# Performance work log

Measured on AMD Instinct MI355X. Metric: run time of the kernel, lower is better.

## Reference

```python
import jax, jax.numpy as jnp
import numpy as np

N = 50000          # nodes
E = 800000         # edges (before self-loops)
IN = 128           # in_dim
HID = 128          # hidden_dim
HEADS = 4
G = 256            # graphs in batch
EPS = 1e-5         # batchnorm eps
NEG_SLOPE = 0.2    # GATConv leaky_relu slope


def _gat_layer(x, src, dst, W, a_src, a_dst, bias, H, C, concat):
    """PyG-style GATConv (self-loops already appended to src/dst)."""
    n = x.shape[0]
    h = (x @ W).reshape(n, H, C)                       # [N,H,C]
    s_src = (h * a_src).sum(-1)                        # [N,H]
    s_dst = (h * a_dst).sum(-1)                        # [N,H]
    e = jax.nn.leaky_relu(s_src[src] + s_dst[dst], NEG_SLOPE)   # [E',H]
    m = jax.ops.segment_max(e, dst, num_segments=n)    # segment-wise softmax
    ex = jnp.exp(e - m[dst])
    den = jax.ops.segment_sum(ex, dst, num_segments=n)
    alpha = ex / den[dst]                              # [E',H]
    out = jax.ops.segment_sum(alpha[..., None] * h[src], dst, num_segments=n)  # [N,H,C]
    out = out.reshape(n, H * C) if concat else out.mean(axis=1)
    return out + bias


def _bn(x, gamma, beta):
    # PyG BatchNorm over nodes (training-mode batch statistics)
    mu = x.mean(axis=0)
    var = x.var(axis=0)
    return gamma * (x - mu) * jax.lax.rsqrt(var + EPS) + beta


def setup_inputs() -> dict:
    key = jax.random.key(0)
    ks = jax.random.split(key, 32)
    d = {}
    d["x"] = jax.random.normal(ks[0], (N, IN), dtype=jnp.float32)
    d["edge_index"] = jax.random.randint(ks[1], (2, E), 0, N, dtype=jnp.int64)
    d["batch_idx"] = jnp.sort(jax.random.randint(ks[2], (N,), 0, G, dtype=jnp.int64))
    dims = [(IN, HEADS, HID, True), (HID * HEADS, HEADS, HID, True), (HID * HEADS, 1, HID, False)]
    for i, (din, H, C, concat) in enumerate(dims):
        d[f"W{i}"] = jax.random.normal(ks[3 + 4 * i], (din, H * C), dtype=jnp.float32) * 0.05
        d[f"att_src{i}"] = jax.random.normal(ks[4 + 4 * i], (H, C), dtype=jnp.float32) * 0.05
        d[f"att_dst{i}"] = jax.random.normal(ks[5 + 4 * i], (H, C), dtype=jnp.float32) * 0.05
        out_w = H * C if concat else C
        d[f"bias{i}"] = jnp.zeros((out_w,), dtype=jnp.float32)
        d[f"gamma{i}"] = jnp.ones((out_w,), dtype=jnp.float32)
        d[f"beta{i}"] = jnp.zeros((out_w,), dtype=jnp.float32)
    return d


def reference(x, edge_index, batch_idx,
              W0, att_src0, att_dst0, bias0, gamma0, beta0,
              W1, att_src1, att_dst1, bias1, gamma1, beta1,
              W2, att_src2, att_dst2, bias2, gamma2, beta2):
    n = x.shape[0]
    loops = jnp.arange(n, dtype=edge_index.dtype)
    src = jnp.concatenate([edge_index[0], loops])
    dst = jnp.concatenate([edge_index[1], loops])
    layers = [
        (W0, att_src0, att_dst0, bias0, gamma0, beta0, HEADS, HID, True),
        (W1, att_src1, att_dst1, bias1, gamma1, beta1, HEADS, HID, True),
        (W2, att_src2, att_dst2, bias2, gamma2, beta2, 1, HID, False),
    ]
    h = x
    for (W, a_s, a_d, b, g, bt, H, C, concat) in layers:
        h = _gat_layer(h, src, dst, W, a_s, a_d, b, H, C, concat)
        h = jax.nn.elu(_bn(h, g, bt))
        # dropout: identity in eval mode
    # global_mean_pool over batch_idx
    sums = jax.ops.segment_sum(h, batch_idx, num_segments=G)
    cnt = jax.ops.segment_sum(jnp.ones((n,), dtype=h.dtype), batch_idx, num_segments=G)
    return sums / jnp.maximum(cnt, 1.0)[:, None]
```

## Files before the change

### kernel.cpp

```cpp
#include <hip/hip_runtime.h>
#include <math.h>
#include <stdint.h>

#define N_NODES 50000
#define N_EDGES 800000
#define EP      (N_EDGES + N_NODES)
#define G_GRAPHS 256
#define BN_EPS   1e-5f
#define NEG_SLOPE 0.2f

typedef short short8 __attribute__((ext_vector_type(8)));
typedef float f32x4 __attribute__((ext_vector_type(4)));
typedef unsigned short u16;

static __device__ __forceinline__ float lrelu(float x) {
    return x > 0.f ? x : NEG_SLOPE * x;
}

static __device__ __forceinline__ u16 bf16hi(float f) {
    unsigned u = __float_as_uint(f);
    u += 0x7FFFu + ((u >> 16) & 1u);
    return (u16)(u >> 16);
}
static __device__ __forceinline__ float bf2f(u16 h) {
    return __uint_as_float((unsigned)h << 16);
}

static __device__ __forceinline__ void gld_lds16(const void* g, void* l) {
    __builtin_amdgcn_global_load_lds((const __attribute__((address_space(1))) void*)g,
                                     (__attribute__((address_space(3))) void*)l, 16, 0, 0);
}

static __device__ __forceinline__ float2 h2f2(unsigned u) {
    union { unsigned u; _Float16 h[2]; } c;
    c.u = u;
    return make_float2((float)c.h[0], (float)c.h[1]);
}

__global__ void k_hist(const int* __restrict__ ei, int* __restrict__ deg) {
    int stride = gridDim.x * blockDim.x;
    for (int e = blockIdx.x * blockDim.x + threadIdx.x; e < EP; e += stride) {
        int d = (e < N_EDGES) ? ei[N_EDGES + e] : (e - N_EDGES);
        atomicAdd(&deg[d], 1);
    }
}

__global__ void k_scan1(const int* __restrict__ deg, int* __restrict__ row_start,
                        int* __restrict__ totals) {
    __shared__ int buf[1024];
    int t = threadIdx.x;
    int i = blockIdx.x * 1024 + t;
    int v = (i < N_NODES) ? deg[i] : 0;
    buf[t] = v;
    __syncthreads();
    for (int off = 1; off < 1024; off <<= 1) {
        int add = (t >= off) ? buf[t - off] : 0;
        __syncthreads();
        buf[t] += add;
        __syncthreads();
    }
    if (i < N_NODES) row_start[i] = buf[t] - v;
    if (t == 1023) totals[blockIdx.x] = buf[t];
}

__global__ void k_scan2(int* __restrict__ totals, int nb) {
    if (threadIdx.x == 0 && blockIdx.x == 0) {
        int run = 0;
        for (int i = 0; i < nb; ++i) { int v = totals[i]; totals[i] = run; run += v; }
    }
}

__global__ void k_scan3(int* __restrict__ row_start, const int* __restrict__ totals) {
    int i = blockIdx.x * blockDim.x + threadIdx.x;
    if (i < N_NODES) row_start[i] += totals[i >> 10];
    if (i == 0) row_start[N_NODES] = EP;
}

__global__ void k_scatter(const int* __restrict__ ei, const int* __restrict__ row_start,
                          int* __restrict__ cursor, int* __restrict__ csr_src) {
    int stride = gridDim.x * blockDim.x;
    for (int e = blockIdx.x * blockDim.x + threadIdx.x; e < EP; e += stride) {
        int s, d;
        if (e < N_EDGES) { s = ei[e]; d = ei[N_EDGES + e]; }
        else             { s = d = e - N_EDGES; }
        int pos = row_start[d] + atomicAdd(&cursor[d], 1);
        csr_src[pos] = s;
    }
}

__global__ void k_cvtW(const float* __restrict__ W, u16* __restrict__ bthi,
                       u16* __restrict__ btlo, int Nc, int nsh, int KS) {
    int i = blockIdx.x * 256 + threadIdx.x;
    if (i >= (KS << 5) * Nc) return;
    int k = i >> nsh;
    int n = i & (Nc - 1);
    int c = n >> 7, col = n & 127;
    int ks = k >> 5, kq = (k >> 3) & 3, j = k & 7;
    size_t idx = ((size_t)(c * KS + ks)) * 4096 + kq * 1024 + col * 8 + j;
    float v = W[i];
    u16 h = bf16hi(v);
    bthi[idx] = h;
    btlo[idx] = bf16hi(v - bf2f(h));
}

__launch_bounds__(256)
__global__ void k_gemm_mfma(const float* __restrict__ A, const u16* __restrict__ bthi,
                            const u16* __restrict__ btlo, _Float16* __restrict__ C2,
                            float* __restrict__ sSg, float* __restrict__ sDg,
                            const float* __restrict__ asr, const float* __restrict__ adr,
                            int M, int K, int Nc) {
    __shared__ u16 Ah[4096], Al[4096], Bh[4096], Bl[4096];
    __shared__ float rS[128], rD[128];
    const int t    = threadIdx.x;
    const int lane = t & 63, wv = t >> 6;
    const int wr = wv >> 1, wc = wv & 1;
    const int lr = lane & 15, kq = lane >> 4;
    const int r0 = blockIdx.x * 128, c0 = blockIdx.y * 128;
    const int KS = K >> 5;
    const int H = Nc >> 7;
    const int head = blockIdx.y;

    const int ar = t >> 1;
    const int ahf = t & 1;
    const int garow = r0 + ar;
    const bool avalid = garow < M;
    const float* arow = A + (size_t)garow * K + ahf * 16;

    const size_t bchunk0 = (size_t)blockIdx.y * KS * 4096;

    f32x4 acc[4][4];
    #pragma unroll
    for (int m = 0; m < 4; ++m)
        #pragma unroll
        for (int n = 0; n < 4; ++n) {
            acc[m][n][0] = 0.f; acc[m][n][1] = 0.f;
            acc[m][n][2] = 0.f; acc[m][n][3] = 0.f;
        }

    for (int ks = 0; ks < KS; ++ks) {
        float4 av[4];
        const float4* ap = (const float4*)(arow + ks * 32);
        if (avalid) {
            av[0] = ap[0]; av[1] = ap[1]; av[2] = ap[2]; av[3] = ap[3];
        } else {
            av[0] = av[1] = av[2] = av[3] = make_float4(0.f, 0.f, 0.f, 0.f);
        }
        __syncthreads();

        float f[16];
        f[0]=av[0].x; f[1]=av[0].y; f[2]=av[0].z; f[3]=av[0].w;
        f[4]=av[1].x; f[5]=av[1].y; f[6]=av[1].z; f[7]=av[1].w;
        f[8]=av[2].x; f[9]=av[2].y; f[10]=av[2].z; f[11]=av[2].w;
        f[12]=av[3].x; f[13]=av[3].y; f[14]=av[3].z; f[15]=av[3].w;
        u16 hi[16], lo[16];
        #pragma unroll
        for (int i = 0; i < 16; ++i) {
            hi[i] = bf16hi(f[i]);
            lo[i] = bf16hi(f[i] - bf2f(hi[i]));
        }
        #pragma unroll
        for (int q = 0; q < 2; ++q) {
            int kqi = ahf * 2 + q;
            int off = kqi * 1024 + ar * 8;
            int4 wh, wl;
            wh.x = (unsigned)hi[q*8+0] | ((unsigned)hi[q*8+1] << 16);
            wh.y = (unsigned)hi[q*8+2] | ((unsigned)hi[q*8+3] << 16);
            wh.z = (unsigned)hi[q*8+4] | ((unsigned)hi[q*8+5] << 16);
            wh.w = (unsigned)hi[q*8+6] | ((unsigned)hi[q*8+7] << 16);
            wl.x = (unsigned)lo[q*8+0] | ((unsigned)lo[q*8+1] << 16);
            wl.y = (unsigned)lo[q*8+2] | ((unsigned)lo[q*8+3] << 16);
            wl.z = (unsigned)lo[q*8+4] | ((unsigned)lo[q*8+5] << 16);
            wl.w = (unsigned)lo[q*8+6] | ((unsigned)lo[q*8+7] << 16);
            *(int4*)&Ah[off] = wh;
            *(int4*)&Al[off] = wl;
        }

        const u16* bhs = bthi + bchunk0 + (size_t)ks * 4096;
        const u16* bls = btlo + bchunk0 + (size_t)ks * 4096;
        #pragma unroll
        for (int p = 0; p < 2; ++p) {
            int ge = p * 2048 + wv * 512 + lane * 8;
            int le = p * 2048 + wv * 512;
            gld_lds16(bhs + ge, &Bh[le]);
            gld_lds16(bls + ge, &Bl[le]);
        }
        __syncthreads();

        short8 afh[4], afl[4], bfh[4], bfl[4];
        #pragma unroll
        for (int m = 0; m < 4; ++m) {
            int row = wr * 64 + m * 16 + lr;
            int off = kq * 1024 + row * 8;
            afh[m] = *(const short8*)&Ah[off];
            afl[m] = *(const short8*)&Al[off];
        }
        #pragma unroll
        for (int n = 0; n < 4; ++n) {
            int col = wc * 64 + n * 16 + lr;
            int off = kq * 1024 + col * 8;
            bfh[n] = *(const short8*)&Bh[off];
            bfl[n] = *(const short8*)&Bl[off];
        }
        #pragma unroll
        for (int m = 0; m < 4; ++m)
            #pragma unroll
            for (int n = 0; n < 4; ++n) {
                acc[m][n] = __builtin_amdgcn_mfma_f32_16x16x32_bf16(afh[m], bfh[n], acc[m][n], 0, 0, 0);
                acc[m][n] = __builtin_amdgcn_mfma_f32_16x16x32_bf16(afh[m], bfl[n], acc[m][n], 0, 0, 0);
                acc[m][n] = __builtin_amdgcn_mfma_f32_16x16x32_bf16(afl[m], bfh[n], acc[m][n], 0, 0, 0);
            }
    }

    float aS[4], aD[4];
    #pragma unroll
    for (int n = 0; n < 4; ++n) {
        int c = c0 + wc * 64 + n * 16 + lr;
        aS[n] = asr[c];
        aD[n] = adr[c];
    }
    __syncthreads();
    if (t < 128) { rS[t] = 0.f; rD[t] = 0.f; }
    __syncthreads();
    #pragma unroll
    for (int m = 0; m < 4; ++m) {
        #pragma unroll
        for (int j = 0; j < 4; ++j) {
            float ps = 0.f, pd = 0.f;
            #pragma unroll
            for (int n = 0; n < 4; ++n) {
                float v = acc[m][n][j];
                ps += v * aS[n];
                pd += v * aD[n];
            }
            #pragma unroll
            for (int off = 1; off < 16; off <<= 1) {
                ps += __shfl_xor(ps, off, 64);
                pd += __shfl_xor(pd, off, 64);
            }
            if (lr == 0) {
                int row = wr * 64 + m * 16 + kq * 4 + j;
                atomicAdd(&rS[row], ps);
                atomicAdd(&rD[row], pd);
            }
        }
    }
    __syncthreads();
    if (t < 128) {
        int r = r0 + t;
        if (r < M) {
            sSg[(size_t)r * H + head] = rS[t];
            sDg[(size_t)r * H + head] = rD[t];
        }
    }

    #pragma unroll
    for (int m = 0; m < 4; ++m) {
        int rowb = r0 + wr * 64 + m * 16 + kq * 4;
        #pragma unroll
        for (int n = 0; n < 4; ++n) {
            int col = c0 + wc * 64 + n * 16 + lr;
            #pragma unroll
            for (int j = 0; j < 4; ++j) {
                int r = rowb + j;
                if (r < M) C2[(size_t)r * Nc + col] = (_Float16)acc[m][n][j];
            }
        }
    }
}

template<int H>
__global__ void k_attn(const float* __restrict__ s_src, const float* __restrict__ s_dst,
                       const int* __restrict__ row_start, const int* __restrict__ csr,
                       float* __restrict__ alpha) {
    int n = blockIdx.x;
    int lane = threadIdx.x;
    const int EPI = 64 / H;
    int head = lane % H;
    int eo   = lane / H;
    int lo = row_start[n], hi = row_start[n + 1];
    float sd = s_dst[n * H + head];

    float mx = -INFINITY;
    for (int p = lo + eo; p < hi; p += EPI) {
        int s = csr[p];
        float e = lrelu(s_src[s * H + head] + sd);
        alpha[(size_t)p * H + head] = e;
        mx = fmaxf(mx, e);
    }
    #pragma unroll
    for (int off = H; off < 64; off <<= 1) mx = fmaxf(mx, __shfl_xor(mx, off, 64));

    float sum = 0.f;
    for (int p = lo + eo; p < hi; p += EPI) {
        float ex = expf(alpha[(size_t)p * H + head] - mx);
        alpha[(size_t)p * H + head] = ex;
        sum += ex;
    }
    #pragma unroll
    for (int off = H; off < 64; off <<= 1) sum += __shfl_xor(sum, off, 64);

    float inv = 1.f / sum;
    for (int p = lo + eo; p < hi; p += EPI) alpha[(size_t)p * H + head] *= inv;
}

template<int H>
__global__ void k_agg2(const _Float16* __restrict__ hb2, const float* __restrict__ alpha,
                       const int* __restrict__ row_start, const int* __restrict__ csr,
                       const float* __restrict__ bias, float* __restrict__ out) {
    const int W = H * 128;
    int n = blockIdx.x;
    int t = threadIdx.x;
    int head = t >> 6;
    int lo = row_start[n], hi = row_start[n + 1];
    float a0 = 0.f, a1 = 0.f;
    int p = lo;
    for (; p + 2 <= hi; p += 2) {
        int s0 = csr[p], s1 = csr[p + 1];
        float al0 = alpha[(size_t)p * H + head];
        float al1 = alpha[(size_t)(p + 1) * H + head];
        unsigned u0 = *(const unsigned*)&hb2[(size_t)s0 * W + 2 * t];
        unsigned u1 = *(const unsigned*)&hb2[(size_t)s1 * W + 2 * t];
        float2 h0 = h2f2(u0), h1 = h2f2(u1);
        a0 += al0 * h0.x + al1 * h1.x;
        a1 += al0 * h0.y + al1 * h1.y;
    }
    if (p < hi) {
        int s0 = csr[p];
        float al0 = alpha[(size_t)p * H + head];
        float2 h0 = h2f2(*(const unsigned*)&hb2[(size_t)s0 * W + 2 * t]);
        a0 += al0 * h0.x;
        a1 += al0 * h0.y;
    }
    out[(size_t)n * W + 2 * t]     = a0 + bias[2 * t];
    out[(size_t)n * W + 2 * t + 1] = a1 + bias[2 * t + 1];
}

__global__ void k_bnstat(const float* __restrict__ x, float* __restrict__ bnsum,
                         float* __restrict__ bnsq, int W) {
    const int RPB = 64;
    int f  = threadIdx.x;
    int r0 = blockIdx.x * RPB;
    int r1 = min(r0 + RPB, N_NODES);
    float s = 0.f, q = 0.f;
    for (int r = r0; r < r1; ++r) {
        float v = x[(size_t)r * W + f];
        s += v; q += v * v;
    }
    atomicAdd(&bnsum[f], s);
    atomicAdd(&bnsq[f], q);
}

__global__ void k_bnelu(float* __restrict__ x, const float* __restrict__ bnsum,
                        const float* __restrict__ bnsq, const float* __restrict__ gamma,
                        const float* __restrict__ beta, int W) {
    size_t total = (size_t)N_NODES * W;
    size_t i = (size_t)blockIdx.x * blockDim.x + threadIdx.x;
    if (i >= total) return;
    int f = (int)(i & (W - 1));
    const float invN = 1.f / (float)N_NODES;
    float mean = bnsum[f] * invN;
    float var  = bnsq[f] * invN - mean * mean;
    float y = gamma[f] * (x[i] - mean) * rsqrtf(var + BN_EPS) + beta[f];
    x[i] = y > 0.f ? y : expm1f(y);
}

__global__ void k_pool(const float* __restrict__ x, const int* __restrict__ batch,
                       float* __restrict__ out) {
    int g = blockIdx.x;
    int f = threadIdx.x;
    int a = 0, b = N_NODES;
    while (a < b) { int m = (a + b) >> 1; if (batch[m] < g) a = m + 1; else b = m; }
    int lo = a;
    b = N_NODES;
    while (a < b) { int m = (a + b) >> 1; if (batch[m] < g + 1) a = m + 1; else b = m; }
    int hi = a;
    float s = 0.f;
    for (int r = lo; r < hi; ++r) s += x[(size_t)r * 128 + f];
    int cnt = hi - lo;
    out[g * 128 + f] = s / (float)(cnt > 0 ? cnt : 1);
}

extern "C" void kernel_launch(void* const* d_in, const int* in_sizes, int n_in,
                              void* d_out, int out_size, void* d_ws, size_t ws_size,
                              hipStream_t stream) {
    const float* x     = (const float*)d_in[0];
    const int*   ei    = (const int*)d_in[1];
    const int*   batch = (const int*)d_in[2];
    const float* Wm[3]  = {(const float*)d_in[3],  (const float*)d_in[9],  (const float*)d_in[15]};
    const float* asr[3] = {(const float*)d_in[4],  (const float*)d_in[10], (const float*)d_in[16]};
    const float* adr[3] = {(const float*)d_in[5],  (const float*)d_in[11], (const float*)d_in[17]};
    const float* bia[3] = {(const float*)d_in[6],  (const float*)d_in[12], (const float*)d_in[18]};
    const float* gam[3] = {(const float*)d_in[7],  (const float*)d_in[13], (const float*)d_in[19]};
    const float* bet[3] = {(const float*)d_in[8],  (const float*)d_in[14], (const float*)d_in[20]};

    char* w = (char*)d_ws;
    auto alloc = [&](size_t bytes) -> void* {
        void* p = (void*)w;
        w += (bytes + 255) & ~(size_t)255;
        return p;
    };
    float*     act = (float*)alloc((size_t)N_NODES * 512 * 4);
    _Float16*  hb2 = (_Float16*)alloc((size_t)N_NODES * 512 * 2);
    float*   alpha = (float*)alloc((size_t)EP * 4 * 4);
    int* csr_src   = (int*)alloc((size_t)EP * 4);
    int* row_start = (int*)alloc((size_t)(N_NODES + 1) * 4);
    int* deg       = (int*)alloc((size_t)N_NODES * 4);
    int* cursor    = (int*)alloc((size_t)N_NODES * 4);
    float* s_src = (float*)alloc((size_t)N_NODES * 4 * 4);
    float* s_dst = (float*)alloc((size_t)N_NODES * 4 * 4);
    float* bn    = (float*)alloc(1024 * 4);
    int* totals  = (int*)alloc(64 * 4);
    u16* bthi = (u16*)alloc((size_t)512 * 512 * 2);
    u16* btlo = (u16*)alloc((size_t)512 * 512 * 2);

    hipMemsetAsync(deg, 0, (size_t)N_NODES * 4, stream);
    hipMemsetAsync(cursor, 0, (size_t)N_NODES * 4, stream);
    k_hist<<<512, 256, 0, stream>>>(ei, deg);
    k_scan1<<<(N_NODES + 1023) / 1024, 1024, 0, stream>>>(deg, row_start, totals);
    k_scan2<<<1, 64, 0, stream>>>(totals, (N_NODES + 1023) / 1024);
    k_scan3<<<(N_NODES + 255) / 256, 256, 0, stream>>>(row_start, totals);
    k_scatter<<<512, 256, 0, stream>>>(ei, row_start, cursor, csr_src);

    auto layer = [&](const float* Ain, int K, int li, int H) {
        int Wd = H * 128;
        int nsh = (Wd == 512) ? 9 : 7;
        int tot = K * Wd;
        k_cvtW<<<(tot + 255) / 256, 256, 0, stream>>>(Wm[li], bthi, btlo, Wd, nsh, K >> 5);
        dim3 gg((N_NODES + 127) / 128, Wd / 128);
        k_gemm_mfma<<<gg, 256, 0, stream>>>(Ain, bthi, btlo, hb2, s_src, s_dst,
                                            asr[li], adr[li], N_NODES, K, Wd);
        if (H == 4) {
            k_attn<4><<<N_NODES, 64, 0, stream>>>(s_src, s_dst, row_start, csr_src, alpha);
            k_agg2<4><<<N_NODES, 256, 0, stream>>>(hb2, alpha, row_start, csr_src, bia[li], act);
        } else {
            k_attn<1><<<N_NODES, 64, 0, stream>>>(s_src, s_dst, row_start, csr_src, alpha);
            k_agg2<1><<<N_NODES, 64, 0, stream>>>(hb2, alpha, row_start, csr_src, bia[li], act);
        }
        hipMemsetAsync(bn, 0, 1024 * 4, stream);
        k_bnstat<<<(N_NODES + 63) / 64, Wd, 0, stream>>>(act, bn, bn + 512, Wd);
        size_t tot2 = (size_t)N_NODES * Wd;
        k_bnelu<<<(unsigned)((tot2 + 255) / 256), 256, 0, stream>>>(act, bn, bn + 512,
                                                                    gam[li], bet[li], Wd);
    };

    layer(x,   128, 0, 4);
    layer(act, 512, 1, 4);
    layer(act, 512, 2, 1);

    k_pool<<<G_GRAPHS, 128, 0, stream>>>(act, batch, (float*)d_out);
}
```

Before: 960.9 us.

## Fuse BatchNorm+ELU into next GEMM load and pool; store activations in fp16

Removes the standalone BN-apply/ELU pass. A tiny kernel now computes per-feature scale and shift, and the normalisation plus ELU is applied while loading A in the next layer's GEMM and inside the final pooling. Aggregation output and activations are stored in fp16 instead of fp32, which halves activation traffic. The alpha layout becomes head-major, and the aggregation processes 4 columns and 4 edges per thread. The risks are reduced precision in the stored pre-BN activations and extra ELU work repeated per GEMM column block.

New measurement: 973.0 us. No clear change (+1.3%).

```diff
diff --git a/kernel.cpp b/kernel.cpp
--- a/kernel.cpp
+++ b/kernel.cpp
@@ -103,11 +103,26 @@
     btlo[idx] = bf16hi(v - bf2f(h));
 }
 
+__global__ void k_bnprep(const float* __restrict__ bnsum, const float* __restrict__ bnsq,
+                         const float* __restrict__ gamma, const float* __restrict__ beta,
+                         float* __restrict__ scale, float* __restrict__ shift, int W) {
+    int f = blockIdx.x * 256 + threadIdx.x;
+    if (f >= W) return;
+    const float invN = 1.f / (float)N_NODES;
+    float mean = bnsum[f] * invN;
+    float var  = bnsq[f] * invN - mean * mean;
+    float sc = gamma[f] * rsqrtf(var + BN_EPS);
+    scale[f] = sc;
+    shift[f] = beta[f] - mean * sc;
+}
+
+template<int AMODE>
 __launch_bounds__(256)
-__global__ void k_gemm_mfma(const float* __restrict__ A, const u16* __restrict__ bthi,
+__global__ void k_gemm_mfma(const void* __restrict__ Av, const u16* __restrict__ bthi,
                             const u16* __restrict__ btlo, _Float16* __restrict__ C2,
                             float* __restrict__ sSg, float* __restrict__ sDg,
                             const float* __restrict__ asr, const float* __restrict__ adr,
+                            const float* __restrict__ scale, const float* __restrict__ shift,
                             int M, int K, int Nc) {
     __shared__ u16 Ah[4096], Al[4096], Bh[4096], Bl[4096];
     __shared__ float rS[128], rD[128];
@@ -124,7 +139,8 @@
     const int ahf = t & 1;
     const int garow = r0 + ar;
     const bool avalid = garow < M;
-    const float* arow = A + (size_t)garow * K + ahf * 16;
+    const float*    arowF = (const float*)Av + (size_t)garow * K + ahf * 16;
+    const _Float16* arowH = (const _Float16*)Av + (size_t)garow * K + ahf * 16;
 
     const size_t bchunk0 = (size_t)blockIdx.y * KS * 4096;
 
@@ -138,20 +154,50 @@
         }
 
     for (int ks = 0; ks < KS; ++ks) {
+        float f[16];
         float4 av[4];
-        const float4* ap = (const float4*)(arow + ks * 32);
-        if (avalid) {
-            av[0] = ap[0]; av[1] = ap[1]; av[2] = ap[2]; av[3] = ap[3];
+        uint4 u0, u1;
+        if constexpr (AMODE == 0) {
+            const float4* ap = (const float4*)(arowF + ks * 32);
+            if (avalid) { av[0] = ap[0]; av[1] = ap[1]; av[2] = ap[2]; av[3] = ap[3]; }
+            else av[0] = av[1] = av[2] = av[3] = make_float4(0.f, 0.f, 0.f, 0.f);
         } else {
-            av[0] = av[1] = av[2] = av[3] = make_float4(0.f, 0.f, 0.f, 0.f);
+            if (avalid) {
+                u0 = *(const uint4*)(arowH + ks * 32);
+                u1 = *(const uint4*)(arowH + ks * 32 + 8);
+            } else {
+                u0.x = u0.y = u0.z = u0.w = 0u;
+                u1.x = u1.y = u1.z = u1.w = 0u;
+            }
         }
         __syncthreads();
 
-        float f[16];
-        f[0]=av[0].x; f[1]=av[0].y; f[2]=av[0].z; f[3]=av[0].w;
-        f[4]=av[1].x; f[5]=av[1].y; f[6]=av[1].z; f[7]=av[1].w;
-        f[8]=av[2].x; f[9]=av[2].y; f[10]=av[2].z; f[11]=av[2].w;
-        f[12]=av[3].x; f[13]=av[3].y; f[14]=av[3].z; f[15]=av[3].w;
+        if constexpr (AMODE == 0) {
+            f[0]=av[0].x; f[1]=av[0].y; f[2]=av[0].z; f[3]=av[0].w;
+            f[4]=av[1].x; f[5]=av[1].y; f[6]=av[1].z; f[7]=av[1].w;
+            f[8]=av[2].x; f[9]=av[2].y; f[10]=av[2].z; f[11]=av[2].w;
+            f[12]=av[3].x; f[13]=av[3].y; f[14]=av[3].z; f[15]=av[3].w;
+        } else {
+            float2 p0 = h2f2(u0.x), p1 = h2f2(u0.y), p2 = h2f2(u0.z), p3 = h2f2(u0.w);
+            float2 p4 = h2f2(u1.x), p5 = h2f2(u1.y), p6 = h2f2(u1.z), p7 = h2f2(u1.w);
+            f[0]=p0.x; f[1]=p0.y; f[2]=p1.x; f[3]=p1.y;
+            f[4]=p2.x; f[5]=p2.y; f[6]=p3.x; f[7]=p3.y;
+            f[8]=p4.x; f[9]=p4.y; f[10]=p5.x; f[11]=p5.y;
+            f[12]=p6.x; f[13]=p6.y; f[14]=p7.x; f[15]=p7.y;
+            const float* scp = scale + ks * 32 + ahf * 16;
+            const float* shp = shift + ks * 32 + ahf * 16;
+            #pragma unroll
+            for (int i = 0; i < 4; ++i) {
+                float4 sc = *(const float4*)(scp + 4 * i);
+                float4 sh = *(const float4*)(shp + 4 * i);
+                float y;
+                y = fmaf(f[4*i+0], sc.x, sh.x); f[4*i+0] = y > 0.f ? y : expm1f(y);
+                y = fmaf(f[4*i+1], sc.y, sh.y); f[4*i+1] = y > 0.f ? y : expm1f(y);
+                y = fmaf(f[4*i+2], sc.z, sh.z); f[4*i+2] = y > 0.f ? y : expm1f(y);
+                y = fmaf(f[4*i+3], sc.w, sh.w); f[4*i+3] = y > 0.f ? y : expm1f(y);
+            }
+        }
+
         u16 hi[16], lo[16];
         #pragma unroll
         for (int i = 0; i < 16; ++i) {
@@ -279,12 +325,13 @@
     int eo   = lane / H;
     int lo = row_start[n], hi = row_start[n + 1];
     float sd = s_dst[n * H + head];
+    float* al = alpha + (size_t)head * EP;
 
     float mx = -INFINITY;
     for (int p = lo + eo; p < hi; p += EPI) {
         int s = csr[p];
         float e = lrelu(s_src[s * H + head] + sd);
-        alpha[(size_t)p * H + head] = e;
+        al[p] = e;
         mx = fmaxf(mx, e);
     }
     #pragma unroll
@@ -292,79 +339,104 @@
 
     float sum = 0.f;
     for (int p = lo + eo; p < hi; p += EPI) {
-        float ex = expf(alpha[(size_t)p * H + head] - mx);
-        alpha[(size_t)p * H + head] = ex;
+        float ex = expf(al[p] - mx);
+        al[p] = ex;
         sum += ex;
     }
     #pragma unroll
     for (int off = H; off < 64; off <<= 1) sum += __shfl_xor(sum, off, 64);
 
     float inv = 1.f / sum;
-    for (int p = lo + eo; p < hi; p += EPI) alpha[(size_t)p * H + head] *= inv;
-}
-
-template<int H>
+    for (int p = lo + eo; p < hi; p += EPI) al[p] *= inv;
+}
+
+template<int H, int CPT>
 __global__ void k_agg2(const _Float16* __restrict__ hb2, const float* __restrict__ alpha,
                        const int* __restrict__ row_start, const int* __restrict__ csr,
-                       const float* __restrict__ bias, float* __restrict__ out) {
+                       const float* __restrict__ bias, _Float16* __restrict__ out) {
     const int W = H * 128;
     int n = blockIdx.x;
     int t = threadIdx.x;
-    int head = t >> 6;
+    int c0 = t * CPT;
+    int head = c0 >> 7;
+    const float* al = alpha + (size_t)head * EP;
     int lo = row_start[n], hi = row_start[n + 1];
-    float a0 = 0.f, a1 = 0.f;
+    float acc[CPT];
+    #pragma unroll
+    for (int j = 0; j < CPT; ++j) acc[j] = 0.f;
+
     int p = lo;
-    for (; p + 2 <= hi; p += 2) {
-        int s0 = csr[p], s1 = csr[p + 1];
-        float al0 = alpha[(size_t)p * H + head];
-        float al1 = alpha[(size_t)(p + 1) * H + head];
-        unsigned u0 = *(const unsigned*)&hb2[(size_t)s0 * W + 2 * t];
-        unsigned u1 = *(const unsigned*)&hb2[(size_t)s1 * W + 2 * t];
-        float2 h0 = h2f2(u0), h1 = h2f2(u1);
-        a0 += al0 * h0.x + al1 * h1.x;
-        a1 += al0 * h0.y + al1 * h1.y;
-    }
-    if (p < hi) {
+    for (; p + 4 <= hi; p += 4) {
+        int s0 = csr[p], s1 = csr[p+1], s2 = csr[p+2], s3 = csr[p+3];
+        float l0 = al[p], l1 = al[p+1], l2 = al[p+2], l3 = al[p+3];
+        if constexpr (CPT == 4) {
+            uint2 v0 = *(const uint2*)&hb2[(size_t)s0 * W + c0];
+            uint2 v1 = *(const uint2*)&hb2[(size_t)s1 * W + c0];
+            uint2 v2 = *(const uint2*)&hb2[(size_t)s2 * W + c0];
+            uint2 v3 = *(const uint2*)&hb2[(size_t)s3 * W + c0];
+            float2 a, b;
+            a = h2f2(v0.x); b = h2f2(v0.y);
+            acc[0] += l0*a.x; acc[1] += l0*a.y; acc[2] += l0*b.x; acc[3] += l0*b.y;
+            a = h2f2(v1.x); b = h2f2(v1.y);
+            acc[0] += l1*a.x; acc[1] += l1*a.y; acc[2] += l1*b.x; acc[3] += l1*b.y;
+            a = h2f2(v2.x); b = h2f2(v2.y);
+            acc[0] += l2*a.x; acc[1] += l2*a.y; acc[2] += l2*b.x; acc[3] += l2*b.y;
+            a = h2f2(v3.x); b = h2f2(v3.y);
+            acc[0] += l3*a.x; acc[1] += l3*a.y; acc[2] += l3*b.x; acc[3] += l3*b.y;
+        } else {
+            unsigned v0 = *(const unsigned*)&hb2[(size_t)s0 * W + c0];
+            unsigned v1 = *(const unsigned*)&hb2[(size_t)s1 * W + c0];
+            unsigned v2 = *(const unsigned*)&hb2[(size_t)s2 * W + c0];
+            unsigned v3 = *(const unsigned*)&hb2[(size_t)s3 * W + c0];
+            float2 a;
+            a = h2f2(v0); acc[0] += l0*a.x; acc[1] += l0*a.y;
+            a = h2f2(v1); acc[0] += l1*a.x; acc[1] += l1*a.y;
+            a = h2f2(v2); acc[0] += l2*a.x; acc[1] += l2*a.y;
+            a = h2f2(v3); acc[0] += l3*a.x; acc[1] += l3*a.y;
+        }
+    }
+    for (; p < hi; ++p) {
         int s0 = csr[p];
-        float al0 = alpha[(size_t)p * H + head];
-        float2 h0 = h2f2(*(const unsigned*)&hb2[(size_t)s0 * W + 2 * t]);
-        a0 += al0 * h0.x;
-        a1 += al0 * h0.y;
-    }
-    out[(size_t)n * W + 2 * t]     = a0 + bias[2 * t];
-    out[(size_t)n * W + 2 * t + 1] = a1 + bias[2 * t + 1];
-}
-
-__global__ void k_bnstat(const float* __restrict__ x, float* __restrict__ bnsum,
-                         float* __restrict__ bnsq, int W) {
+        float l0 = al[p];
+        if constexpr (CPT == 4) {
+            uint2 v0 = *(const uint2*)&hb2[(size_t)s0 * W + c0];
+            float2 a = h2f2(v0.x), b = h2f2(v0.y);
+            acc[0] += l0*a.x; acc[1] += l0*a.y; acc[2] += l0*b.x; acc[3] += l0*b.y;
+        } else {
+            float2 a = h2f2(*(const unsigned*)&hb2[(size_t)s0 * W + c0]);
+            acc[0] += l0*a.x; acc[1] += l0*a.y;
+        }
+    }
+
+    union { _Float16 h[CPT]; unsigned u[CPT/2]; } pk;
+    #pragma unroll
+    for (int j = 0; j < CPT; ++j) pk.h[j] = (_Float16)(acc[j] + bias[c0 + j]);
+    if constexpr (CPT == 4)
+        *(uint2*)&out[(size_t)n * W + c0] = *(uint2*)pk.u;
+    else
+        *(unsigned*)&out[(size_t)n * W + c0] = pk.u[0];
+}
+
+__global__ void k_bnstat2(const _Float16* __restrict__ x, float* __restrict__ bnsum,
+                          float* __restrict__ bnsq, int W) {
     const int RPB = 64;
-    int f  = threadIdx.x;
+    int t  = threadIdx.x;
     int r0 = blockIdx.x * RPB;
     int r1 = min(r0 + RPB, N_NODES);
-    float s = 0.f, q = 0.f;
+    float s0 = 0.f, q0 = 0.f, s1 = 0.f, q1 = 0.f;
     for (int r = r0; r < r1; ++r) {
-        float v = x[(size_t)r * W + f];
-        s += v; q += v * v;
-    }
-    atomicAdd(&bnsum[f], s);
-    atomicAdd(&bnsq[f], q);
-}
-
-__global__ void k_bnelu(float* __restrict__ x, const float* __restrict__ bnsum,
-                        const float* __restrict__ bnsq, const float* __restrict__ gamma,
-                        const float* __restrict__ beta, int W) {
-    size_t total = (size_t)N_NODES * W;
-    size_t i = (size_t)blockIdx.x * blockDim.x + threadIdx.x;
-    if (i >= total) return;
-    int f = (int)(i & (W - 1));
-    const float invN = 1.f / (float)N_NODES;
-    float mean = bnsum[f] * invN;
-    float var  = bnsq[f] * invN - mean * mean;
-    float y = gamma[f] * (x[i] - mean) * rsqrtf(var + BN_EPS) + beta[f];
-    x[i] = y > 0.f ? y : expm1f(y);
-}
-
-__global__ void k_pool(const float* __restrict__ x, const int* __restrict__ batch,
+        float2 v = h2f2(*(const unsigned*)&x[(size_t)r * W + 2 * t]);
+        s0 += v.x; q0 += v.x * v.x;
+        s1 += v.y; q1 += v.y * v.y;
+    }
+    atomicAdd(&bnsum[2*t],   s0);
+    atomicAdd(&bnsq[2*t],    q0);
+    atomicAdd(&bnsum[2*t+1], s1);
+    atomicAdd(&bnsq[2*t+1],  q1);
+}
+
+__global__ void k_pool(const _Float16* __restrict__ x, const int* __restrict__ batch,
+                       const float* __restrict__ scale, const float* __restrict__ shift,
                        float* __restrict__ out) {
     int g = blockIdx.x;
     int f = threadIdx.x;
@@ -374,8 +446,13 @@
     b = N_NODES;
     while (a < b) { int m = (a + b) >> 1; if (batch[m] < g + 1) a = m + 1; else b = m; }
     int hi = a;
+    float sc = scale[f], sh = shift[f];
     float s = 0.f;
-    for (int r = lo; r < hi; ++r) s += x[(size_t)r * 128 + f];
+    for (int r = lo; r < hi; ++r) {
+        float v = (float)x[(size_t)r * 128 + f];
+        float y = fmaf(v, sc, sh);
+        s += (y > 0.f) ? y : expm1f(y);
+    }
     int cnt = hi - lo;
     out[g * 128 + f] = s / (float)(cnt > 0 ? cnt : 1);
 }
@@ -399,8 +476,9 @@
         w += (bytes + 255) & ~(size_t)255;
         return p;
     };
-    float*     act = (float*)alloc((size_t)N_NODES * 512 * 4);
-    _Float16*  hb2 = (_Float16*)alloc((size_t)N_NODES * 512 * 2);
+    _Float16* act2   = (_Float16*)alloc((size_t)N_NODES * 512 * 2);
+    _Float16* act128 = (_Float16*)alloc((size_t)N_NODES * 128 * 2);
+    _Float16* hb2    = (_Float16*)alloc((size_t)N_NODES * 512 * 2);
     float*   alpha = (float*)alloc((size_t)EP * 4 * 4);
     int* csr_src   = (int*)alloc((size_t)EP * 4);
     int* row_start = (int*)alloc((size_t)(N_NODES + 1) * 4);
@@ -409,6 +487,8 @@
     float* s_src = (float*)alloc((size_t)N_NODES * 4 * 4);
     float* s_dst = (float*)alloc((size_t)N_NODES * 4 * 4);
     float* bn    = (float*)alloc(1024 * 4);
+    float* scl   = (float*)alloc(512 * 4);
+    float* shf   = (float*)alloc(512 * 4);
     int* totals  = (int*)alloc(64 * 4);
     u16* bthi = (u16*)alloc((size_t)512 * 512 * 2);
     u16* btlo = (u16*)alloc((size_t)512 * 512 * 2);
@@ -421,31 +501,33 @@
     k_scan3<<<(N_NODES + 255) / 256, 256, 0, stream>>>(row_start, totals);
     k_scatter<<<512, 256, 0, stream>>>(ei, row_start, cursor, csr_src);
 
-    auto layer = [&](const float* Ain, int K, int li, int H) {
+    auto layer = [&](const void* Ain, int K, int li, int H, int amode, _Float16* outAct) {
         int Wd = H * 128;
         int nsh = (Wd == 512) ? 9 : 7;
         int tot = K * Wd;
         k_cvtW<<<(tot + 255) / 256, 256, 0, stream>>>(Wm[li], bthi, btlo, Wd, nsh, K >> 5);
         dim3 gg((N_NODES + 127) / 128, Wd / 128);
-        k_gemm_mfma<<<gg, 256, 0, stream>>>(Ain, bthi, btlo, hb2, s_src, s_dst,
-                                            asr[li], adr[li], N_NODES, K, Wd);
+        if (amode == 0)
+            k_gemm_mfma<0><<<gg, 256, 0, stream>>>(Ain, bthi, btlo, hb2, s_src, s_dst,
+                                                   asr[li], adr[li], scl, shf, N_NODES, K, Wd);
+        else
+            k_gemm_mfma<1><<<gg, 256, 0, stream>>>(Ain, bthi, btlo, hb2, s_src, s_dst,
+                                                   asr[li], adr[li], scl, shf, N_NODES, K, Wd);
         if (H == 4) {
             k_attn<4><<<N_NODES, 64, 0, stream>>>(s_src, s_dst, row_start, csr_src, alpha);
-            k_agg2<4><<<N_NODES, 256, 0, stream>>>(hb2, alpha, row_start, csr_src, bia[li], act);
+            k_agg2<4, 4><<<N_NODES, 128, 0, stream>>>(hb2, alpha, row_start, csr_src, bia[li], outAct);
         } else {
             k_attn<1><<<N_NODES, 64, 0, stream>>>(s_src, s_dst, row_start, csr_src, alpha);
-            k_agg2<1><<<N_NODES, 64, 0, stream>>>(hb2, alpha, row_start, csr_src, bia[li], act);
+            k_agg2<1, 2><<<N_NODES, 64, 0, stream>>>(hb2, alpha, row_start, csr_src, bia[li], outAct);
         }
         hipMemsetAsync(bn, 0, 1024 * 4, stream);
-        k_bnstat<<<(N_NODES + 63) / 64, Wd, 0, stream>>>(act, bn, bn + 512, Wd);
-        size_t tot2 = (size_t)N_NODES * Wd;
-        k_bnelu<<<(unsigned)((tot2 + 255) / 256), 256, 0, stream>>>(act, bn, bn + 512,
-                                                                    gam[li], bet[li], Wd);
+        k_bnstat2<<<(N_NODES + 63) / 64, Wd / 2, 0, stream>>>(outAct, bn, bn + 512, Wd);
+        k_bnprep<<<(Wd + 255) / 256, 256, 0, stream>>>(bn, bn + 512, gam[li], bet[li], scl, shf, Wd);
     };
 
-    layer(x,   128, 0, 4);
-    layer(act, 512, 1, 4);
-    layer(act, 512, 2, 1);
-
-    k_pool<<<G_GRAPHS, 128, 0, stream>>>(act, batch, (float*)d_out);
-}
+    layer(x,    128, 0, 4, 0, act2);
+    layer(act2, 512, 1, 4, 1, act2);
+    layer(act2, 512, 2, 1, 1, act128);
+
+    k_pool<<<G_GRAPHS, 128, 0, stream>>>(act128, batch, scl, shf, (float*)d_out);
+}
```
